# Kernel optimization log

Measured on AMD Instinct MI355X. Metric: run time of the kernel, lower is better.

Reference implementation:

```python
import jax, jax.numpy as jnp
import numpy as np

CS = 256
CT = 256
RED = 4


def _mlp(x, w1, b1, w2, b2):
    # Linear -> ReLU -> Linear -> Sigmoid (torch Linear: y = x @ W.T + b)
    h = jax.nn.relu(x @ w1.T + b1)
    return jax.nn.sigmoid(h @ w2.T + b2)


def _row_normalize(g, eps=1e-12):
    # F.normalize(g, p=2, dim=1)
    n = jnp.sqrt(jnp.sum(g * g, axis=1, keepdims=True))
    return g / jnp.maximum(n, eps)


def setup_inputs() -> dict:
    key = jax.random.key(0)
    ks = jax.random.split(key, 32)
    B, C, H, W = 128, 256, 28, 28
    inp = {
        'student': jax.random.normal(ks[0], (B, C, H, W), jnp.float32),
        'teacher': jax.random.normal(ks[1], (B, C, H, W), jnp.float32),
    }
    hid_cat = (CS + CT) // RED  # 128
    hid_s = CS // RED           # 64
    hid_t = CT // RED           # 64
    specs = [
        ('fc_s', CS + CT, hid_cat, CS),
        ('fc_s_add', CS, hid_s, CS),
        ('fc_s_mul', CS, hid_s, CS),
        ('fc_t', CS + CT, hid_cat, CT),
        ('fc_t_add', CT, hid_t, CT),
        ('fc_t_mul', CT, hid_t, CT),
    ]
    i = 2
    for name, din, dh, dout in specs:
        inp[name + '_w1'] = jax.random.normal(ks[i], (dh, din), jnp.float32) * 0.05
        inp[name + '_b1'] = jnp.zeros((dh,), jnp.float32)
        inp[name + '_w2'] = jax.random.normal(ks[i + 1], (dout, dh), jnp.float32) * 0.05
        inp[name + '_b2'] = jnp.zeros((dout,), jnp.float32)
        i += 2
    return inp


def reference(student, teacher,
              fc_s_w1, fc_s_b1, fc_s_w2, fc_s_b2,
              fc_s_add_w1, fc_s_add_b1, fc_s_add_w2, fc_s_add_b2,
              fc_s_mul_w1, fc_s_mul_b1, fc_s_mul_w2, fc_s_mul_b2,
              fc_t_w1, fc_t_b1, fc_t_w2, fc_t_b2,
              fc_t_add_w1, fc_t_add_b1, fc_t_add_w2, fc_t_add_b2,
              fc_t_mul_w1, fc_t_mul_b1, fc_t_mul_w2, fc_t_mul_b2):
    b_s, c_s = student.shape[0], student.shape[1]
    b_t, c_t = teacher.shape[0], teacher.shape[1]

    fm_s = student.reshape(b_s, -1)                 # [B, C*H*W]
    G_s = fm_s @ fm_s.T                             # [B, B]
    norm_G_s = _row_normalize(G_s)
    y_s = jnp.mean(student, axis=(2, 3))            # adaptive avg pool -> [B, C]

    fm_t = teacher.reshape(b_t, -1)
    G_t = fm_t @ fm_t.T
    norm_G_t = _row_normalize(G_t)
    y_t = jnp.mean(teacher, axis=(2, 3))

    zs = norm_G_s @ y_s                             # [B, c_s]
    zt = norm_G_t @ y_t                             # [B, c_t]
    z_add = zs + zt
    z_mul = zs * zt
    z = jnp.concatenate([zs, zt], axis=1)           # [B, c_s + c_t]

    g_s = _mlp(z, fc_s_w1, fc_s_b1, fc_s_w2, fc_s_b2)
    g_s_add = _mlp(z_add, fc_s_add_w1, fc_s_add_b1, fc_s_add_w2, fc_s_add_b2)
    g_s_mul = _mlp(z_mul, fc_s_mul_w1, fc_s_mul_b1, fc_s_mul_w2, fc_s_mul_b2)
    g_t = _mlp(z, fc_t_w1, fc_t_b1, fc_t_w2, fc_t_b2)
    g_t_add = _mlp(z_add, fc_t_add_w1, fc_t_add_b1, fc_t_add_w2, fc_t_add_b2)
    g_t_mul = _mlp(z_mul, fc_t_mul_w1, fc_t_mul_b1, fc_t_mul_w2, fc_t_mul_b2)

    # relu is a no-op after sigmoid but kept for faithfulness
    gate_s = (jax.nn.relu(g_s) + jax.nn.relu(g_s_add) + jax.nn.relu(g_s_mul))[:, :, None, None]
    gate_t = (jax.nn.relu(g_t) + jax.nn.relu(g_t_add) + jax.nn.relu(g_t_mul))[:, :, None, None]
    return gate_s * student, gate_t * teacher
```

## Files before the change

kernel.cpp:

```cpp
#include <hip/hip_runtime.h>


typedef __bf16 bf16x8 __attribute__((ext_vector_type(8)));
typedef __bf16 bf16x4 __attribute__((ext_vector_type(4)));
typedef float f32x4 __attribute__((ext_vector_type(4)));
typedef unsigned short ushortx8 __attribute__((ext_vector_type(8)));

#define LSTR 136

__device__ __forceinline__ bf16x8 ldfrag(const unsigned short* p) {
    return __builtin_bit_cast(bf16x8, *reinterpret_cast<const ushortx8*>(p));
}

__global__ __launch_bounds__(256, 2) void k_gram(
    const float* __restrict__ student, const float* __restrict__ teacher,
    float* __restrict__ partials,
    float* __restrict__ y_ws)
{
    const int blk = blockIdx.x;
    const int tensor = blk >> 8;
    const int ch = blk & 255;
    const float* __restrict__ src = tensor ? teacher : student;

    const int tid = threadIdx.x;
    const int wave = tid >> 6;
    const int lane = tid & 63;
    const int mrow = lane & 15;
    const int koff = (lane >> 4) * 8;

    __shared__ unsigned short lds[128 * LSTR];

    const int r = tid >> 1;
    const int half = tid & 1;

    {
        ushortx8 zz = {0, 0, 0, 0, 0, 0, 0, 0};
        *reinterpret_cast<ushortx8*>(&lds[r * LSTR + 112 + 8 * half]) = zz;
    }

    const float4* srow = reinterpret_cast<const float4*>(
        src + (size_t)r * 200704 + (size_t)ch * 784 + half * 56);
    unsigned short* dst = &lds[r * LSTR + half * 56];

    f32x4 acc[2][8];
    f32x4 zv = {0.f, 0.f, 0.f, 0.f};
#pragma unroll
    for (int a = 0; a < 2; ++a)
#pragma unroll
        for (int b = 0; b < 8; ++b) acc[a][b] = zv;

    float msum = 0.f;

    float4 v[14];
#pragma unroll
    for (int j = 0; j < 14; ++j) v[j] = srow[j];

    for (int t = 0; t < 7; ++t) {
#pragma unroll
        for (int j = 0; j < 14; ++j) {
            float4 w = v[j];
            msum += (w.x + w.y) + (w.z + w.w);
            bf16x4 hv = {(__bf16)w.x, (__bf16)w.y, (__bf16)w.z, (__bf16)w.w};
            *reinterpret_cast<bf16x4*>(dst + 4 * j) = hv;
        }
        __syncthreads();

        if (t < 6) {
#pragma unroll
            for (int j = 0; j < 14; ++j) v[j] = srow[(t + 1) * 28 + j];
        }

#pragma unroll
        for (int kk = 0; kk < 4; ++kk) {
            const int col = kk * 32 + koff;
            bf16x8 a0 = ldfrag(&lds[(32 * wave + mrow) * LSTR + col]);
            bf16x8 a1 = ldfrag(&lds[(32 * wave + 16 + mrow) * LSTR + col]);
#pragma unroll
            for (int nt = 0; nt < 8; ++nt) {
                bf16x8 bb = ldfrag(&lds[(16 * nt + mrow) * LSTR + col]);
                acc[0][nt] = __builtin_amdgcn_mfma_f32_16x16x32_bf16(a0, bb, acc[0][nt], 0, 0, 0);
                acc[1][nt] = __builtin_amdgcn_mfma_f32_16x16x32_bf16(a1, bb, acc[1][nt], 0, 0, 0);
            }
        }
        __syncthreads();
    }

    float other = __shfl_xor(msum, 1);
    if (half == 0)
        y_ws[tensor * 32768 + r * 256 + ch] = (msum + other) * (1.f / 784.f);

    const int crow = (lane >> 4) * 4;
    const int ccol = lane & 15;
    const size_t blkoff = (size_t)blk * 128;
#pragma unroll
    for (int rt = 0; rt < 2; ++rt)
#pragma unroll
        for (int nt = 0; nt < 8; ++nt)
#pragma unroll
            for (int g = 0; g < 4; ++g) {
                int m = 32 * wave + 16 * rt + crow + g;
                int n = 16 * nt + ccol;
                partials[((size_t)m << 16) + blkoff + n] = acc[rt][nt][g];
            }
}

__device__ __forceinline__ float sigm(float x) { return 1.f / (1.f + __expf(-x)); }

__device__ __forceinline__ float dotf4(const float* a, const float* __restrict__ b, int n4) {
    const float4* a4 = reinterpret_cast<const float4*>(a);
    const float4* b4 = reinterpret_cast<const float4*>(b);
    float s = 0.f;
    for (int d = 0; d < n4; ++d) {
        float4 x = a4[d], y = b4[d];
        s += x.x * y.x + x.y * y.y + x.z * y.z + x.w * y.w;
    }
    return s;
}

__global__ __launch_bounds__(256) void k_gates(
    const float* __restrict__ partials, const float* __restrict__ y_ws,
    float* __restrict__ gates,
    const float* __restrict__ fs_w1, const float* __restrict__ fs_b1,
    const float* __restrict__ fs_w2, const float* __restrict__ fs_b2,
    const float* __restrict__ fsa_w1, const float* __restrict__ fsa_b1,
    const float* __restrict__ fsa_w2, const float* __restrict__ fsa_b2,
    const float* __restrict__ fsm_w1, const float* __restrict__ fsm_b1,
    const float* __restrict__ fsm_w2, const float* __restrict__ fsm_b2,
    const float* __restrict__ ft_w1, const float* __restrict__ ft_b1,
    const float* __restrict__ ft_w2, const float* __restrict__ ft_b2,
    const float* __restrict__ fta_w1, const float* __restrict__ fta_b1,
    const float* __restrict__ fta_w2, const float* __restrict__ fta_b2,
    const float* __restrict__ ftm_w1, const float* __restrict__ ftm_b1,
    const float* __restrict__ ftm_w2, const float* __restrict__ ftm_b2)
{
    const int b = blockIdx.x;
    const int tid = threadIdx.x;
    const int wave = tid >> 6;
    const int lane = tid & 63;

    __shared__ __align__(16) float Gn[2][128];
    __shared__ float wred[4];
    __shared__ __align__(16) float z[512];
    __shared__ __align__(16) float za[256];
    __shared__ __align__(16) float zm[256];
    __shared__ __align__(16) float hbuf[256];
    __shared__ __align__(16) float h2buf[256];
    __shared__ __align__(16) float red[8][128];

    {
        const int pg = tid >> 5;
        const int jq = tid & 31;
        const float4* pb4 = reinterpret_cast<const float4*>(partials + ((size_t)b << 16))
                            + (size_t)(pg * 64) * 32 + jq;
        float4 s = {0.f, 0.f, 0.f, 0.f};
#pragma unroll 8
        for (int p = 0; p < 64; ++p) {
            float4 vv = pb4[p * 32];
            s.x += vv.x; s.y += vv.y; s.z += vv.z; s.w += vv.w;
        }
        *reinterpret_cast<float4*>(&red[pg][jq * 4]) = s;
    }
    __syncthreads();

    const int tt = tid >> 7;
    const int j = tid & 127;
    float g = (red[tt * 4 + 0][j] + red[tt * 4 + 1][j]) +
              (red[tt * 4 + 2][j] + red[tt * 4 + 3][j]);

    float v2 = g * g;
#pragma unroll
    for (int off = 32; off > 0; off >>= 1) v2 += __shfl_xor(v2, off);
    if (lane == 0) wred[wave] = v2;
    __syncthreads();
    float ss = tt ? (wred[2] + wred[3]) : (wred[0] + wred[1]);
    float inv = 1.f / fmaxf(sqrtf(ss), 1e-12f);
    Gn[tt][j] = g * inv;
    __syncthreads();

    const int c = tid;
    float zs = 0.f, zt = 0.f;
    const float* ys = y_ws;
    const float* yt = y_ws + 32768;
    for (int jj = 0; jj < 128; ++jj) {
        zs = fmaf(Gn[0][jj], ys[jj * 256 + c], zs);
        zt = fmaf(Gn[1][jj], yt[jj * 256 + c], zt);
    }
    z[c] = zs;
    z[256 + c] = zt;
    za[c] = zs + zt;
    zm[c] = zs * zt;
    __syncthreads();

    {
        const int h = tid & 127;
        const float* w = (tid < 128) ? (fs_w1 + h * 512) : (ft_w1 + h * 512);
        const float* bb = (tid < 128) ? fs_b1 : ft_b1;
        hbuf[tid] = fmaxf(bb[h] + dotf4(z, w, 128), 0.f);
    }
    {
        const int q = tid >> 6;
        const int i = tid & 63;
        const float* w = (q == 0) ? fsa_w1 : (q == 1) ? fta_w1 : (q == 2) ? fsm_w1 : ftm_w1;
        const float* bb = (q == 0) ? fsa_b1 : (q == 1) ? fta_b1 : (q == 2) ? fsm_b1 : ftm_b1;
        const float* in = (q < 2) ? za : zm;
        h2buf[tid] = fmaxf(bb[i] + dotf4(in, w + i * 256, 64), 0.f);
    }
    __syncthreads();

    {
        float gs  = sigm(fs_b2[c]  + dotf4(hbuf,        fs_w2  + c * 128, 32));
        float gt  = sigm(ft_b2[c]  + dotf4(hbuf + 128,  ft_w2  + c * 128, 32));
        float gsa = sigm(fsa_b2[c] + dotf4(h2buf,       fsa_w2 + c * 64, 16));
        float gta = sigm(fta_b2[c] + dotf4(h2buf + 64,  fta_w2 + c * 64, 16));
        float gsm = sigm(fsm_b2[c] + dotf4(h2buf + 128, fsm_w2 + c * 64, 16));
        float gtm = sigm(ftm_b2[c] + dotf4(h2buf + 192, ftm_w2 + c * 64, 16));
        gates[b * 256 + c] = gs + gsa + gsm;
        gates[32768 + b * 256 + c] = gt + gta + gtm;
    }
}

__global__ __launch_bounds__(256) void k_apply(
    const float4* __restrict__ student4, const float4* __restrict__ teacher4,
    const float* __restrict__ gates, float* __restrict__ out)
{
    const unsigned i = blockIdx.x * 256u + threadIdx.x;
    const unsigned PER = 6422528u;
    const unsigned isT = (i >= PER) ? 1u : 0u;
    const unsigned jj = i - isT * PER;
    const unsigned bc = jj / 196u;
    const float g = gates[isT * 32768u + bc];
    const float4* in = isT ? teacher4 : student4;
    float4 v = in[jj];
    f32x4 r = {v.x * g, v.y * g, v.z * g, v.w * g};
    __builtin_nontemporal_store(r, reinterpret_cast<f32x4*>(out) + i);
}

extern "C" void kernel_launch(void* const* d_in, const int* in_sizes, int n_in,
                              void* d_out, int out_size, void* d_ws, size_t ws_size,
                              hipStream_t stream) {
    (void)in_sizes; (void)n_in; (void)out_size; (void)ws_size;

    const float* student = (const float*)d_in[0];
    const float* teacher = (const float*)d_in[1];
    const float* fs_w1  = (const float*)d_in[2];
    const float* fs_b1  = (const float*)d_in[3];
    const float* fs_w2  = (const float*)d_in[4];
    const float* fs_b2  = (const float*)d_in[5];
    const float* fsa_w1 = (const float*)d_in[6];
    const float* fsa_b1 = (const float*)d_in[7];
    const float* fsa_w2 = (const float*)d_in[8];
    const float* fsa_b2 = (const float*)d_in[9];
    const float* fsm_w1 = (const float*)d_in[10];
    const float* fsm_b1 = (const float*)d_in[11];
    const float* fsm_w2 = (const float*)d_in[12];
    const float* fsm_b2 = (const float*)d_in[13];
    const float* ft_w1  = (const float*)d_in[14];
    const float* ft_b1  = (const float*)d_in[15];
    const float* ft_w2  = (const float*)d_in[16];
    const float* ft_b2  = (const float*)d_in[17];
    const float* fta_w1 = (const float*)d_in[18];
    const float* fta_b1 = (const float*)d_in[19];
    const float* fta_w2 = (const float*)d_in[20];
    const float* fta_b2 = (const float*)d_in[21];
    const float* ftm_w1 = (const float*)d_in[22];
    const float* ftm_b1 = (const float*)d_in[23];
    const float* ftm_w2 = (const float*)d_in[24];
    const float* ftm_b2 = (const float*)d_in[25];

    float* out = (float*)d_out;
    float* partials = out;
    float* y_ws = (float*)d_ws;
    float* gates = y_ws + 65536;

    k_gram<<<dim3(512), dim3(256), 0, stream>>>(student, teacher, partials, y_ws);
    k_gates<<<dim3(128), dim3(256), 0, stream>>>(partials, y_ws, gates,
        fs_w1, fs_b1, fs_w2, fs_b2,
        fsa_w1, fsa_b1, fsa_w2, fsa_b2,
        fsm_w1, fsm_b1, fsm_w2, fsm_b2,
        ft_w1, ft_b1, ft_w2, ft_b2,
        fta_w1, fta_b1, fta_w2, fta_b2,
        ftm_w1, ftm_b1, ftm_w2, ftm_b2);
    k_apply<<<dim3(50176), dim3(256), 0, stream>>>(
        (const float4*)student, (const float4*)teacher, gates, out);
}
```

Before: 479.2 us.

## Process two channels per gram block with double-buffered LDS pipelining

```diff
diff --git a/kernel.cpp b/kernel.cpp
--- a/kernel.cpp
+++ b/kernel.cpp
@@ -12,14 +12,14 @@
     return __builtin_bit_cast(bf16x8, *reinterpret_cast<const ushortx8*>(p));
 }
 
-__global__ __launch_bounds__(256, 2) void k_gram(
+__global__ __launch_bounds__(256, 1) void k_gram(
     const float* __restrict__ student, const float* __restrict__ teacher,
     float* __restrict__ partials,
     float* __restrict__ y_ws)
 {
     const int blk = blockIdx.x;
-    const int tensor = blk >> 8;
-    const int ch = blk & 255;
+    const int tensor = blk >> 7;
+    const int chpair = blk & 127;
     const float* __restrict__ src = tensor ? teacher : student;
 
     const int tid = threadIdx.x;
@@ -28,19 +28,23 @@
     const int mrow = lane & 15;
     const int koff = (lane >> 4) * 8;
 
-    __shared__ unsigned short lds[128 * LSTR];
+    __shared__ unsigned short lds[2][128 * LSTR];
 
     const int r = tid >> 1;
     const int half = tid & 1;
 
     {
         ushortx8 zz = {0, 0, 0, 0, 0, 0, 0, 0};
-        *reinterpret_cast<ushortx8*>(&lds[r * LSTR + 112 + 8 * half]) = zz;
-    }
-
-    const float4* srow = reinterpret_cast<const float4*>(
-        src + (size_t)r * 200704 + (size_t)ch * 784 + half * 56);
-    unsigned short* dst = &lds[r * LSTR + half * 56];
+        *reinterpret_cast<ushortx8*>(&lds[0][r * LSTR + 112 + 8 * half]) = zz;
+        *reinterpret_cast<ushortx8*>(&lds[1][r * LSTR + 112 + 8 * half]) = zz;
+    }
+
+    const float4* s0 = reinterpret_cast<const float4*>(
+        src + (size_t)r * 200704 + (size_t)(2 * chpair) * 784 + half * 56);
+    const float4* s1 = reinterpret_cast<const float4*>(
+        src + (size_t)r * 200704 + (size_t)(2 * chpair + 1) * 784 + half * 56);
+    unsigned short* dst0 = &lds[0][r * LSTR + half * 56];
+    unsigned short* dst1 = &lds[1][r * LSTR + half * 56];
 
     f32x4 acc[2][8];
     f32x4 zv = {0.f, 0.f, 0.f, 0.f};
@@ -49,45 +53,72 @@
 #pragma unroll
         for (int b = 0; b < 8; ++b) acc[a][b] = zv;
 
-    float msum = 0.f;
-
-    float4 v[14];
-#pragma unroll
-    for (int j = 0; j < 14; ++j) v[j] = srow[j];
-
-    for (int t = 0; t < 7; ++t) {
-#pragma unroll
-        for (int j = 0; j < 14; ++j) {
-            float4 w = v[j];
-            msum += (w.x + w.y) + (w.z + w.w);
-            bf16x4 hv = {(__bf16)w.x, (__bf16)w.y, (__bf16)w.z, (__bf16)w.w};
-            *reinterpret_cast<bf16x4*>(dst + 4 * j) = hv;
-        }
+    float msum0 = 0.f, msum1 = 0.f;
+
+    float4 vE[14], vO[14];
+
+#define ISSUE(vv, t)                                                        \
+    {                                                                       \
+        const float4* base_ = ((t) < 7 ? s0 : s1) + ((t) < 7 ? (t) : (t)-7) * 28; \
+        _Pragma("unroll")                                                   \
+        for (int j = 0; j < 14; ++j) (vv)[j] = base_[j];                    \
+    }
+
+#define CVTW(vv, dstp, t)                                                   \
+    {                                                                       \
+        float* ms_ = ((t) < 7) ? &msum0 : &msum1;                           \
+        _Pragma("unroll")                                                   \
+        for (int j = 0; j < 14; ++j) {                                      \
+            float4 w = (vv)[j];                                             \
+            *ms_ += (w.x + w.y) + (w.z + w.w);                              \
+            bf16x4 hv = {(__bf16)w.x, (__bf16)w.y, (__bf16)w.z, (__bf16)w.w}; \
+            *reinterpret_cast<bf16x4*>((dstp) + 4 * j) = hv;                \
+        }                                                                   \
+    }
+
+#define MFMA_TILE(buf)                                                      \
+    {                                                                       \
+        const unsigned short* b_ = (buf);                                   \
+        _Pragma("unroll")                                                   \
+        for (int kk = 0; kk < 4; ++kk) {                                    \
+            const int col = kk * 32 + koff;                                 \
+            bf16x8 a0 = ldfrag(&b_[(32 * wave + mrow) * LSTR + col]);       \
+            bf16x8 a1 = ldfrag(&b_[(32 * wave + 16 + mrow) * LSTR + col]);  \
+            _Pragma("unroll")                                               \
+            for (int nt = 0; nt < 8; ++nt) {                                \
+                bf16x8 bb = ldfrag(&b_[(16 * nt + mrow) * LSTR + col]);     \
+                acc[0][nt] = __builtin_amdgcn_mfma_f32_16x16x32_bf16(a0, bb, acc[0][nt], 0, 0, 0); \
+                acc[1][nt] = __builtin_amdgcn_mfma_f32_16x16x32_bf16(a1, bb, acc[1][nt], 0, 0, 0); \
+            }                                                               \
+        }                                                                   \
+    }
+
+    ISSUE(vE, 0);
+    ISSUE(vO, 1);
+    CVTW(vE, dst0, 0);
+    __syncthreads();
+
+#pragma unroll
+    for (int tp = 0; tp < 14; tp += 2) {
+        if (tp + 2 < 14) ISSUE(vE, tp + 2);
+        CVTW(vO, dst1, tp + 1);
+        MFMA_TILE(&lds[0][0]);
         __syncthreads();
-
-        if (t < 6) {
-#pragma unroll
-            for (int j = 0; j < 14; ++j) v[j] = srow[(t + 1) * 28 + j];
-        }
-
-#pragma unroll
-        for (int kk = 0; kk < 4; ++kk) {
-            const int col = kk * 32 + koff;
-            bf16x8 a0 = ldfrag(&lds[(32 * wave + mrow) * LSTR + col]);
-            bf16x8 a1 = ldfrag(&lds[(32 * wave + 16 + mrow) * LSTR + col]);
-#pragma unroll
-            for (int nt = 0; nt < 8; ++nt) {
-                bf16x8 bb = ldfrag(&lds[(16 * nt + mrow) * LSTR + col]);
-                acc[0][nt] = __builtin_amdgcn_mfma_f32_16x16x32_bf16(a0, bb, acc[0][nt], 0, 0, 0);
-                acc[1][nt] = __builtin_amdgcn_mfma_f32_16x16x32_bf16(a1, bb, acc[1][nt], 0, 0, 0);
-            }
-        }
+        if (tp + 3 < 14) ISSUE(vO, tp + 3);
+        if (tp + 2 < 14) CVTW(vE, dst0, tp + 2);
+        MFMA_TILE(&lds[1][0]);
         __syncthreads();
     }
-
-    float other = __shfl_xor(msum, 1);
-    if (half == 0)
-        y_ws[tensor * 32768 + r * 256 + ch] = (msum + other) * (1.f / 784.f);
+#undef ISSUE
+#undef CVTW
+#undef MFMA_TILE
+
+    float o0 = __shfl_xor(msum0, 1);
+    float o1 = __shfl_xor(msum1, 1);
+    if (half == 0) {
+        y_ws[tensor * 32768 + r * 256 + 2 * chpair]     = (msum0 + o0) * (1.f / 784.f);
+        y_ws[tensor * 32768 + r * 256 + 2 * chpair + 1] = (msum1 + o1) * (1.f / 784.f);
+    }
 
     const int crow = (lane >> 4) * 4;
     const int ccol = lane & 15;
@@ -100,7 +131,7 @@
             for (int g = 0; g < 4; ++g) {
                 int m = 32 * wave + 16 * rt + crow + g;
                 int n = 16 * nt + ccol;
-                partials[((size_t)m << 16) + blkoff + n] = acc[rt][nt][g];
+                partials[((size_t)m << 15) + blkoff + n] = acc[rt][nt][g];
             }
 }
 
@@ -150,11 +181,11 @@
     {
         const int pg = tid >> 5;
         const int jq = tid & 31;
-        const float4* pb4 = reinterpret_cast<const float4*>(partials + ((size_t)b << 16))
-                            + (size_t)(pg * 64) * 32 + jq;
+        const float4* pb4 = reinterpret_cast<const float4*>(partials)
+                            + (size_t)b * 8192 + pg * 1024 + jq;
         float4 s = {0.f, 0.f, 0.f, 0.f};
 #pragma unroll 8
-        for (int p = 0; p < 64; ++p) {
+        for (int p = 0; p < 32; ++p) {
             float4 vv = pb4[p * 32];
             s.x += vv.x; s.y += vv.y; s.z += vv.z; s.w += vv.w;
         }
@@ -272,7 +303,7 @@
     float* y_ws = (float*)d_ws;
     float* gates = y_ws + 65536;
 
-    k_gram<<<dim3(512), dim3(256), 0, stream>>>(student, teacher, partials, y_ws);
+    k_gram<<<dim3(256), dim3(256), 0, stream>>>(student, teacher, partials, y_ws);
     k_gates<<<dim3(128), dim3(256), 0, stream>>>(partials, y_ws, gates,
         fs_w1, fs_b1, fs_w2, fs_b2,
         fsa_w1, fsa_b1, fsa_w2, fsa_b2,
```

Result: no change. 477.0 us (-0.5%).
